# Performance work log

Hardware: AMD Instinct MI355X
Metric: run time of the kernel (lower is better)

The kernel has to match this reference:

```python
import jax, jax.numpy as jnp
import numpy as np

N, D, H, E_RAW = 100000, 128, 8, 1600000
C = D // H  # head dim = 16
NEG_SLOPE = 0.2
LN_EPS = 1e-5


def _glorot(key, shape):
    fan_in, fan_out = shape[0], shape[-1]
    lim = (6.0 / (fan_in + fan_out)) ** 0.5
    return jax.random.uniform(key, shape, jnp.float32, -lim, lim)


def setup_inputs() -> dict:
    key = jax.random.key(0)
    ks = jax.random.split(key, 16)
    inp = {
        "x": jax.random.normal(ks[0], (N, D), jnp.float32),
        "edge_index": jax.random.randint(ks[1], (2, E_RAW), 0, N, jnp.int64),
    }
    for l in range(2):
        o = 2 + 4 * l
        inp[f"Wl{l}"] = _glorot(ks[o + 0], (D, H * C))
        inp[f"Wr{l}"] = _glorot(ks[o + 1], (D, H * C))
        inp[f"att{l}"] = _glorot(ks[o + 2], (H, C))
        inp[f"b{l}"] = jnp.zeros((H * C,), jnp.float32)
        inp[f"g{l}"] = jnp.ones((D,), jnp.float32)
        inp[f"beta{l}"] = jnp.zeros((D,), jnp.float32)
    return inp


def _gatv2_layer(x, src, dst, Wl, Wr, att, b):
    # GATv2Conv: e_ij = att . leaky_relu(Wl x_j + Wr x_i); softmax over j -> i
    xl = (x @ Wl).reshape(N, H, C)  # source transform
    xr = (x @ Wr).reshape(N, H, C)  # target transform
    m = jax.nn.leaky_relu(xl[src] + xr[dst], NEG_SLOPE)  # [E,H,C]
    e = jnp.einsum("ehc,hc->eh", m, att)  # [E,H]
    emax = jax.ops.segment_max(e, dst, num_segments=N)[dst]
    ex = jnp.exp(e - emax)
    denom = jax.ops.segment_sum(ex, dst, num_segments=N)[dst]
    alpha = ex / denom  # per-destination softmax
    out = jax.ops.segment_sum(xl[src] * alpha[:, :, None], dst, num_segments=N)
    return out.reshape(N, H * C) + b


def _layernorm(x, g, beta):
    mu = jnp.mean(x, axis=-1, keepdims=True)
    var = jnp.var(x, axis=-1, keepdims=True)
    return (x - mu) * jax.lax.rsqrt(var + LN_EPS) * g + beta


def reference(x, edge_index, Wl0, Wr0, att0, b0, g0, beta0,
              Wl1, Wr1, att1, b1, g1, beta1):
    # add_self_loops=True (PyG default): every node attends to itself
    loop = jnp.arange(N, dtype=edge_index.dtype)
    src = jnp.concatenate([edge_index[0], loop])
    dst = jnp.concatenate([edge_index[1], loop])
    params = [(Wl0, Wr0, att0, b0, g0, beta0), (Wl1, Wr1, att1, b1, g1, beta1)]
    for Wl, Wr, att, b, g, beta in params:
        residual = x
        h = _gatv2_layer(x, src, dst, Wl, Wr, att, b)  # dropout is identity (eval)
        h = jax.nn.elu(h)
        x = _layernorm(h + residual, g, beta)
    return x
```

## Files before the change

### kernel.cpp

```cpp
#include <hip/hip_runtime.h>
#include <cstdint>

#define LEAKY 0.2f
#define LN_EPS 1e-5f

typedef __attribute__((ext_vector_type(8))) short short8;
typedef __attribute__((ext_vector_type(4))) float f32x4;
typedef __attribute__((ext_vector_type(2))) float f32x2;

__device__ __forceinline__ ushort bf16_rne(float x) {
    unsigned u = __float_as_uint(x);
    unsigned r = (u + 0x7fffu + ((u >> 16) & 1u)) >> 16;
    return (ushort)r;
}
__device__ __forceinline__ float bf16_to_f(ushort h) {
    return __uint_as_float(((unsigned)h) << 16);
}
__device__ __forceinline__ f32x2 unpk(uint u) {
    f32x2 r;
    r.x = __uint_as_float(u << 16);
    r.y = __uint_as_float(u & 0xffff0000u);
    return r;
}
__device__ __forceinline__ uint cvt_pk_bf16(float lo, float hi) {
    uint r;
    asm("v_cvt_pk_bf16_f32 %0, %1, %2" : "=v"(r) : "v"(lo), "v"(hi));
    return r;
}
template <int CTRL>
__device__ __forceinline__ float dpp_radd(float v) {
    int sh = __builtin_amdgcn_update_dpp(0, __float_as_int(v), CTRL, 0xF, 0xF, true);
    return v + __int_as_float(sh);
}

__global__ void hist_part(const int* __restrict__ ei, int er, int etot, int n,
                          int* __restrict__ deg) {
    const int xcd = blockIdx.x & 7;
    const int lo = (int)((long long)n * xcd >> 3);
    const int hi = (int)((long long)n * (xcd + 1) >> 3);
    const int stride = (gridDim.x >> 3) * blockDim.x;
    for (int e = (blockIdx.x >> 3) * blockDim.x + threadIdx.x; e < etot;
         e += stride) {
        int dst = (e < er) ? ei[er + e] : (e - er);
        if (dst >= lo && dst < hi) atomicAdd(&deg[dst], 1);
    }
}

__global__ void fill_part(const int* __restrict__ ei, int er, int etot, int n,
                          int* __restrict__ offs, int* __restrict__ colv) {
    const int xcd = blockIdx.x & 7;
    const int lo = (int)((long long)n * xcd >> 3);
    const int hi = (int)((long long)n * (xcd + 1) >> 3);
    const int stride = (gridDim.x >> 3) * blockDim.x;
    for (int e = (blockIdx.x >> 3) * blockDim.x + threadIdx.x; e < etot;
         e += stride) {
        int dst = (e < er) ? ei[er + e] : (e - er);
        if (dst >= lo && dst < hi) {
            int src = (e < er) ? ei[e] : dst;
            int pos = atomicAdd(&offs[dst], 1);
            colv[pos] = src;
        }
    }
}

__global__ __launch_bounds__(1024) void scanA(const int* __restrict__ deg,
                                              int* __restrict__ escan,
                                              int* __restrict__ bsum, int n) {
    __shared__ int wsum[16], wpre[16];
    const int lane = threadIdx.x & 63, wv = threadIdx.x >> 6;
    const int i = blockIdx.x * 1024 + threadIdx.x;
    int v = (i < n) ? deg[i] : 0;
    int x = v;
#pragma unroll
    for (int off = 1; off < 64; off <<= 1) {
        int y = __shfl_up(x, off, 64);
        if (lane >= off) x += y;
    }
    if (lane == 63) wsum[wv] = x;
    __syncthreads();
    if (wv == 0) {
        int s = (lane < 16) ? wsum[lane] : 0;
#pragma unroll
        for (int off = 1; off < 16; off <<= 1) {
            int y = __shfl_up(s, off, 64);
            if (lane >= off) s += y;
        }
        if (lane < 16) wpre[lane] = s;
    }
    __syncthreads();
    int excl = x - v + (wv ? wpre[wv - 1] : 0);
    if (i < n) escan[i] = excl;
    if (threadIdx.x == 1023) bsum[blockIdx.x] = wpre[15];
}

__global__ __launch_bounds__(1024) void scanB(const int* __restrict__ bsum,
                                              int* __restrict__ bpre, int nb) {
    __shared__ int wsum[16], wpre[16];
    const int lane = threadIdx.x & 63, wv = threadIdx.x >> 6;
    const int i = threadIdx.x;
    int v = (i < nb) ? bsum[i] : 0;
    int x = v;
#pragma unroll
    for (int off = 1; off < 64; off <<= 1) {
        int y = __shfl_up(x, off, 64);
        if (lane >= off) x += y;
    }
    if (lane == 63) wsum[wv] = x;
    __syncthreads();
    if (wv == 0) {
        int s = (lane < 16) ? wsum[lane] : 0;
#pragma unroll
        for (int off = 1; off < 16; off <<= 1) {
            int y = __shfl_up(s, off, 64);
            if (lane >= off) s += y;
        }
        if (lane < 16) wpre[lane] = s;
    }
    __syncthreads();
    if (i < nb) bpre[i] = x - v + (wv ? wpre[wv - 1] : 0);
}

__global__ void scanC(const int* __restrict__ escan, const int* __restrict__ bpre,
                      int* __restrict__ offs, int n) {
    int i = blockIdx.x * 256 + threadIdx.x;
    if (i >= n) return;
    offs[i] = escan[i] + bpre[i >> 10];
}

__global__ void cvt_w2(const float* __restrict__ Wl0, const float* __restrict__ Wr0,
                       const float* __restrict__ Wl1, const float* __restrict__ Wr1,
                       ushort* __restrict__ Whi, ushort* __restrict__ Wlo) {
    int t = blockIdx.x * 256 + threadIdx.x;
    int layer = t >> 15;
    int i = t & 32767;
    int colblk = i >> 11;
    int ks = (i >> 9) & 3;
    int lane = (i >> 3) & 63;
    int j = i & 7;
    int col = colblk * 16 + (lane & 15);
    int k = ks * 32 + (lane >> 4) * 8 + j;
    const float* Wl = layer ? Wl1 : Wl0;
    const float* Wr = layer ? Wr1 : Wr0;
    float v = (col < 128) ? Wl[(size_t)k * 128 + col]
                          : Wr[(size_t)k * 128 + (col - 128)];
    ushort h = bf16_rne(v);
    Whi[t] = h;
    Wlo[t] = bf16_rne(v - bf16_to_f(h));
}

template <bool ABF16>
__global__ __launch_bounds__(256) void gemm_mfma(
    const void* __restrict__ Xin,
    const ushort* __restrict__ Wfhi, const ushort* __restrict__ Wflo,
    uint* __restrict__ Olb, uint* __restrict__ Orb, int nrows) {
    __shared__ float4 xs[64 * 32];
    const int t = threadIdx.x;
    const int wave = t >> 6, lane = t & 63;
    const int m0 = blockIdx.x * 64;
    if (ABF16) {
        const uint4* Xv = (const uint4*)Xin + (size_t)m0 * 16;
        uint4* xsb = (uint4*)xs;
#pragma unroll
        for (int i = 0; i < 4; ++i) {
            int idx = i * 256 + t;
            int row = idx >> 4, kc = idx & 15;
            uint4 v = {0u, 0u, 0u, 0u};
            if (m0 + row < nrows) v = Xv[idx];
            xsb[row * 16 + (kc ^ (row & 7))] = v;
        }
    } else {
        const float4* Xv = (const float4*)Xin + (size_t)m0 * 32;
#pragma unroll
        for (int i = 0; i < 8; ++i) {
            int idx = i * 256 + t;
            int row = idx >> 5, kc = idx & 31;
            float4 v = {0.f, 0.f, 0.f, 0.f};
            if (m0 + row < nrows) v = Xv[idx];
            xs[row * 32 + (kc ^ (row & 7))] = v;
        }
    }
    __syncthreads();

    const int lrow = lane & 15;
    const int lkc = (lane >> 4) * 2;
    f32x4 acc[4][4];
#pragma unroll
    for (int mt = 0; mt < 4; ++mt)
#pragma unroll
        for (int nt = 0; nt < 4; ++nt) acc[mt][nt] = (f32x4){0.f, 0.f, 0.f, 0.f};

#pragma unroll 1
    for (int ks = 0; ks < 4; ++ks) {
        short8 bhi[4], blo[4];
#pragma unroll
        for (int nt = 0; nt < 4; ++nt) {
            size_t off = (((size_t)(wave * 4 + nt) * 4 + ks) * 64 + lane) * 8;
            bhi[nt] = *(const short8*)&Wfhi[off];
            blo[nt] = *(const short8*)&Wflo[off];
        }
        short8 ahi[4];
#pragma unroll
        for (int mt = 0; mt < 4; ++mt) {
            const int row = mt * 16 + lrow;
            if (ABF16) {
                const int slot = ks * 4 + (lane >> 4);
                uint4 w = ((const uint4*)xs)[row * 16 + (slot ^ (row & 7))];
                ahi[mt] = *(const short8*)&w;
            } else {
                const int kc0 = ks * 8 + lkc;
                float4 v0 = xs[row * 32 + (kc0 ^ (row & 7))];
                float4 v1 = xs[row * 32 + ((kc0 + 1) ^ (row & 7))];
                uint4 q;
                q.x = cvt_pk_bf16(v0.x, v0.y);
                q.y = cvt_pk_bf16(v0.z, v0.w);
                q.z = cvt_pk_bf16(v1.x, v1.y);
                q.w = cvt_pk_bf16(v1.z, v1.w);
                ahi[mt] = *(const short8*)&q;
            }
        }
#pragma unroll
        for (int nt = 0; nt < 4; ++nt) {
#pragma unroll
            for (int mt = 0; mt < 4; ++mt) {
                acc[mt][nt] = __builtin_amdgcn_mfma_f32_16x16x32_bf16(
                    ahi[mt], blo[nt], acc[mt][nt], 0, 0, 0);
                acc[mt][nt] = __builtin_amdgcn_mfma_f32_16x16x32_bf16(
                    ahi[mt], bhi[nt], acc[mt][nt], 0, 0, 0);
            }
        }
    }
    uint* __restrict__ O = (wave < 2) ? Olb : Orb;
    const int cbase = (wave * 64) & 127;
    const int crow0 = (lane >> 4) * 4;
    const bool evn = (lane & 1) == 0;
#pragma unroll
    for (int mt = 0; mt < 4; ++mt) {
#pragma unroll
        for (int i = 0; i < 4; ++i) {
            const int row = m0 + mt * 16 + crow0 + i;
#pragma unroll
            for (int nt = 0; nt < 4; ++nt) {
                float val = acc[mt][nt][i];
                float pv = __shfl_xor(val, 1);
                uint pk = (uint)bf16_rne(val) | ((uint)bf16_rne(pv) << 16);
                if (evn && row < nrows) {
                    const int col = cbase + nt * 16 + lrow;
                    O[(size_t)row * 64 + (col >> 1)] = pk;
                }
            }
        }
    }
}

template <bool RBF16, bool OBF16>
__global__ __launch_bounds__(256) void gat_agg(
    const uint* __restrict__ xl, const uint* __restrict__ xr,
    const int* __restrict__ offs, const int* __restrict__ colv,
    const float* __restrict__ att,
    const float* __restrict__ bias, const float* __restrict__ gamma,
    const float* __restrict__ beta, const void* __restrict__ resid,
    void* __restrict__ out, int nnode) {
    const int lane = threadIdx.x & 63;
    const int wid = __builtin_amdgcn_readfirstlane(threadIdx.x >> 6);
    const int wave0 = blockIdx.x * 4 + wid;
    const int wstride = gridDim.x * 4;
    const f32x2 att2 = ((const f32x2*)att)[lane];
    const f32x2 b2 = ((const f32x2*)bias)[lane];
    const f32x2 g2 = ((const f32x2*)gamma)[lane];
    const f32x2 be2 = ((const f32x2*)beta)[lane];
    for (int gid = wave0; gid < nnode; gid += wstride) {
        const uint xru = __builtin_nontemporal_load(xr + (size_t)gid * 64 + lane);
        const f32x2 xr2 = unpk(xru);
        float den = 0.f;
        f32x2 acc = {0.f, 0.f};
        int e = gid ? offs[gid - 1] : 0;
        const int e1 = offs[gid];
        for (; e + 4 <= e1; e += 4) {
            int s[4];
#pragma unroll
            for (int k = 0; k < 4; ++k)
                s[k] = __builtin_amdgcn_readfirstlane(colv[e + k]);
            uint u[4];
#pragma unroll
            for (int k = 0; k < 4; ++k) u[k] = xl[(size_t)s[k] * 64 + lane];
#pragma unroll
            for (int k = 0; k < 4; ++k) {
                f32x2 a = unpk(u[k]);
                f32x2 m = a + xr2;
                f32x2 l = m * LEAKY;
                m.x = fmaxf(m.x, l.x); m.y = fmaxf(m.y, l.y);
                f32x2 t = m * att2;
                float p = t.x + t.y;
                p = dpp_radd<0xB1>(p);
                p = dpp_radd<0x4E>(p);
                p = dpp_radd<0x141>(p);
                float ex = __expf(p);
                den += ex;
                acc += a * ex;
            }
        }
        for (; e < e1; ++e) {
            int s0 = __builtin_amdgcn_readfirstlane(colv[e]);
            uint u0 = xl[(size_t)s0 * 64 + lane];
            f32x2 a0 = unpk(u0);
            f32x2 m0 = a0 + xr2;
            f32x2 l0 = m0 * LEAKY;
            m0.x = fmaxf(m0.x, l0.x); m0.y = fmaxf(m0.y, l0.y);
            f32x2 t0 = m0 * att2;
            float p0 = t0.x + t0.y;
            p0 = dpp_radd<0xB1>(p0);
            p0 = dpp_radd<0x4E>(p0);
            p0 = dpp_radd<0x141>(p0);
            float ex0 = __expf(p0);
            den += ex0;
            acc += a0 * ex0;
        }
        const float inv_den = 1.f / den;
        f32x2 v = acc * inv_den + b2;
        v.x = v.x > 0.f ? v.x : expm1f(v.x);
        v.y = v.y > 0.f ? v.y : expm1f(v.y);
        f32x2 r2;
        if (RBF16) {
            uint ru = __builtin_nontemporal_load(
                (const uint*)resid + (size_t)gid * 64 + lane);
            r2 = unpk(ru);
        } else {
            r2 = __builtin_nontemporal_load(
                (const f32x2*)resid + (size_t)gid * 64 + lane);
        }
        f32x2 tv = v + r2;
        float s = tv.x + tv.y, ss = tv.x * tv.x + tv.y * tv.y;
        s = dpp_radd<0xB1>(s);   ss = dpp_radd<0xB1>(ss);
        s = dpp_radd<0x4E>(s);   ss = dpp_radd<0x4E>(ss);
        s = dpp_radd<0x141>(s);  ss = dpp_radd<0x141>(ss);
        s = dpp_radd<0x140>(s);  ss = dpp_radd<0x140>(ss);
        s += __shfl_xor(s, 16);  ss += __shfl_xor(ss, 16);
        s += __shfl_xor(s, 32);  ss += __shfl_xor(ss, 32);
        const float mu = s * 0.0078125f;
        const float var = ss * 0.0078125f - mu * mu;
        const float iv = rsqrtf(var + LN_EPS);
        f32x2 o = (tv - mu) * iv * g2 + be2;
        if (OBF16) {
            uint po = (uint)bf16_rne(o.x) | ((uint)bf16_rne(o.y) << 16);
            __builtin_nontemporal_store(po, (uint*)out + (size_t)gid * 64 + lane);
        } else {
            __builtin_nontemporal_store(o, (f32x2*)out + (size_t)gid * 64 + lane);
        }
    }
}

extern "C" void kernel_launch(void* const* d_in, const int* in_sizes, int n_in,
                              void* d_out, int out_size, void* d_ws, size_t ws_size,
                              hipStream_t stream) {
    const float* x   = (const float*)d_in[0];
    const int*   ei  = (const int*)d_in[1];
    const float* Wl0 = (const float*)d_in[2];
    const float* Wr0 = (const float*)d_in[3];
    const float* at0 = (const float*)d_in[4];
    const float* b0  = (const float*)d_in[5];
    const float* g0  = (const float*)d_in[6];
    const float* be0 = (const float*)d_in[7];
    const float* Wl1 = (const float*)d_in[8];
    const float* Wr1 = (const float*)d_in[9];
    const float* at1 = (const float*)d_in[10];
    const float* b1  = (const float*)d_in[11];
    const float* g1  = (const float*)d_in[12];
    const float* be1 = (const float*)d_in[13];

    const int NF = in_sizes[0];
    const int n  = NF / 128;
    const int er = in_sizes[1] / 2;
    const int etot = er + n;
    const int nb = (n + 1023) / 1024;

    uint* A     = (uint*)d_ws;
    uint* B     = A + (size_t)NF / 2;
    uint* C1    = B + (size_t)NF / 2;
    ushort* Whi = (ushort*)(C1 + (size_t)NF / 2);
    ushort* Wlo = Whi + 65536;
    int* deg    = (int*)(Wlo + 65536);
    int* offs   = deg + n;
    int* escan  = offs + (n + 4);
    int* bsum   = escan + n;
    int* bpre   = bsum + 1024;
    int* colv   = bpre + 1024;
    float* C    = (float*)d_out;

    (void)hipMemsetAsync(deg, 0, (size_t)n * sizeof(int), stream);
    hist_part<<<2048, 256, 0, stream>>>(ei, er, etot, n, deg);
    scanA<<<nb, 1024, 0, stream>>>(deg, escan, bsum, n);
    scanB<<<1, 1024, 0, stream>>>(bsum, bpre, nb);
    scanC<<<(n + 255) / 256, 256, 0, stream>>>(escan, bpre, offs, n);
    fill_part<<<2048, 256, 0, stream>>>(ei, er, etot, n, offs, colv);
    cvt_w2<<<256, 256, 0, stream>>>(Wl0, Wr0, Wl1, Wr1, Whi, Wlo);

    const int gblk = (n + 63) / 64;

    gemm_mfma<false><<<gblk, 256, 0, stream>>>(x, Whi, Wlo, A, B, n);
    gat_agg<false, true><<<2048, 256, 0, stream>>>(
        A, B, offs, colv, at0, b0, g0, be0, x, C1, n);
    gemm_mfma<true><<<gblk, 256, 0, stream>>>(C1, Whi + 32768, Wlo + 32768,
                                              A, B, n);
    gat_agg<true, false><<<2048, 256, 0, stream>>>(
        A, B, offs, colv, at1, b1, g1, be1, C1, C, n);
}
```

Measured before the change: 449.0 us.

## Split each wave into two half-waves processing different edges in the aggregation kernel

The GAT aggregation kernel now has each 32-lane half-wave cover the full 128-feature row with 4 features per lane. The two halves process different neighbor edges at once, two per half per iteration, using 8-byte gathers. Partial softmax sums are combined across halves with a cross-half shuffle at the end, and one half writes the output. This doubles the number of edge gathers in flight per wave and shortens the per-edge dot-product reduction. The costs are masked work on tail iterations, extra cross-half shuffles, and idle lanes during the store.

```diff
diff --git a/kernel.cpp b/kernel.cpp
--- a/kernel.cpp
+++ b/kernel.cpp
@@ -7,6 +7,7 @@
 typedef __attribute__((ext_vector_type(8))) short short8;
 typedef __attribute__((ext_vector_type(4))) float f32x4;
 typedef __attribute__((ext_vector_type(2))) float f32x2;
+typedef __attribute__((ext_vector_type(2))) uint u32x2;
 
 __device__ __forceinline__ ushort bf16_rne(float x) {
     unsigned u = __float_as_uint(x);
@@ -16,10 +17,12 @@
 __device__ __forceinline__ float bf16_to_f(ushort h) {
     return __uint_as_float(((unsigned)h) << 16);
 }
-__device__ __forceinline__ f32x2 unpk(uint u) {
-    f32x2 r;
-    r.x = __uint_as_float(u << 16);
-    r.y = __uint_as_float(u & 0xffff0000u);
+__device__ __forceinline__ f32x4 unpk4(u32x2 u) {
+    f32x4 r;
+    r.x = __uint_as_float(u.x << 16);
+    r.y = __uint_as_float(u.x & 0xffff0000u);
+    r.z = __uint_as_float(u.y << 16);
+    r.w = __uint_as_float(u.y & 0xffff0000u);
     return r;
 }
 __device__ __forceinline__ uint cvt_pk_bf16(float lo, float hi) {
@@ -261,90 +264,100 @@
     const float* __restrict__ beta, const void* __restrict__ resid,
     void* __restrict__ out, int nnode) {
     const int lane = threadIdx.x & 63;
+    const int hl = lane & 31;
+    const int half = lane >> 5;
     const int wid = __builtin_amdgcn_readfirstlane(threadIdx.x >> 6);
     const int wave0 = blockIdx.x * 4 + wid;
     const int wstride = gridDim.x * 4;
-    const f32x2 att2 = ((const f32x2*)att)[lane];
-    const f32x2 b2 = ((const f32x2*)bias)[lane];
-    const f32x2 g2 = ((const f32x2*)gamma)[lane];
-    const f32x2 be2 = ((const f32x2*)beta)[lane];
+    const f32x4 att4 = ((const f32x4*)att)[hl];
+    const f32x4 b4 = ((const f32x4*)bias)[hl];
+    const f32x4 g4 = ((const f32x4*)gamma)[hl];
+    const f32x4 be4 = ((const f32x4*)beta)[hl];
+    const u32x2* __restrict__ xl2 = (const u32x2*)xl;
     for (int gid = wave0; gid < nnode; gid += wstride) {
-        const uint xru = __builtin_nontemporal_load(xr + (size_t)gid * 64 + lane);
-        const f32x2 xr2 = unpk(xru);
+        const u32x2 xru = __builtin_nontemporal_load(
+            (const u32x2*)xr + (size_t)gid * 32 + hl);
+        const f32x4 xr4 = unpk4(xru);
         float den = 0.f;
-        f32x2 acc = {0.f, 0.f};
+        f32x4 acc = {0.f, 0.f, 0.f, 0.f};
         int e = gid ? offs[gid - 1] : 0;
         const int e1 = offs[gid];
-        for (; e + 4 <= e1; e += 4) {
-            int s[4];
-#pragma unroll
-            for (int k = 0; k < 4; ++k)
-                s[k] = __builtin_amdgcn_readfirstlane(colv[e + k]);
-            uint u[4];
-#pragma unroll
-            for (int k = 0; k < 4; ++k) u[k] = xl[(size_t)s[k] * 64 + lane];
-#pragma unroll
-            for (int k = 0; k < 4; ++k) {
-                f32x2 a = unpk(u[k]);
-                f32x2 m = a + xr2;
-                f32x2 l = m * LEAKY;
-                m.x = fmaxf(m.x, l.x); m.y = fmaxf(m.y, l.y);
-                f32x2 t = m * att2;
-                float p = t.x + t.y;
-                p = dpp_radd<0xB1>(p);
-                p = dpp_radd<0x4E>(p);
-                p = dpp_radd<0x141>(p);
-                float ex = __expf(p);
-                den += ex;
-                acc += a * ex;
-            }
-        }
-        for (; e < e1; ++e) {
+        const int e1m = e1 - 1;
+        for (; e < e1; e += 4) {
             int s0 = __builtin_amdgcn_readfirstlane(colv[e]);
-            uint u0 = xl[(size_t)s0 * 64 + lane];
-            f32x2 a0 = unpk(u0);
-            f32x2 m0 = a0 + xr2;
-            f32x2 l0 = m0 * LEAKY;
-            m0.x = fmaxf(m0.x, l0.x); m0.y = fmaxf(m0.y, l0.y);
-            f32x2 t0 = m0 * att2;
-            float p0 = t0.x + t0.y;
-            p0 = dpp_radd<0xB1>(p0);
-            p0 = dpp_radd<0x4E>(p0);
-            p0 = dpp_radd<0x141>(p0);
-            float ex0 = __expf(p0);
-            den += ex0;
-            acc += a0 * ex0;
-        }
+            int s1 = __builtin_amdgcn_readfirstlane(colv[min(e + 1, e1m)]);
+            int s2 = __builtin_amdgcn_readfirstlane(colv[min(e + 2, e1m)]);
+            int s3 = __builtin_amdgcn_readfirstlane(colv[min(e + 3, e1m)]);
+            int selA = half ? s1 : s0;
+            int selB = half ? s3 : s2;
+            u32x2 uA = xl2[(size_t)selA * 32 + hl];
+            u32x2 uB = xl2[(size_t)selB * 32 + hl];
+            f32x4 aA = unpk4(uA);
+            f32x4 mA = aA + xr4;
+            mA.x = fmaxf(mA.x, LEAKY * mA.x); mA.y = fmaxf(mA.y, LEAKY * mA.y);
+            mA.z = fmaxf(mA.z, LEAKY * mA.z); mA.w = fmaxf(mA.w, LEAKY * mA.w);
+            f32x4 tA = mA * att4;
+            float pA = (tA.x + tA.y) + (tA.z + tA.w);
+            pA = dpp_radd<0xB1>(pA);
+            pA = dpp_radd<0x4E>(pA);
+            float exA = (e + half < e1) ? __expf(pA) : 0.f;
+            den += exA;
+            acc += aA * exA;
+            f32x4 aB = unpk4(uB);
+            f32x4 mB = aB + xr4;
+            mB.x = fmaxf(mB.x, LEAKY * mB.x); mB.y = fmaxf(mB.y, LEAKY * mB.y);
+            mB.z = fmaxf(mB.z, LEAKY * mB.z); mB.w = fmaxf(mB.w, LEAKY * mB.w);
+            f32x4 tB = mB * att4;
+            float pB = (tB.x + tB.y) + (tB.z + tB.w);
+            pB = dpp_radd<0xB1>(pB);
+            pB = dpp_radd<0x4E>(pB);
+            float exB = (e + 2 + half < e1) ? __expf(pB) : 0.f;
+            den += exB;
+            acc += aB * exB;
+        }
+        den += __shfl_xor(den, 32);
+        acc.x += __shfl_xor(acc.x, 32);
+        acc.y += __shfl_xor(acc.y, 32);
+        acc.z += __shfl_xor(acc.z, 32);
+        acc.w += __shfl_xor(acc.w, 32);
         const float inv_den = 1.f / den;
-        f32x2 v = acc * inv_den + b2;
+        f32x4 v = acc * inv_den + b4;
         v.x = v.x > 0.f ? v.x : expm1f(v.x);
         v.y = v.y > 0.f ? v.y : expm1f(v.y);
-        f32x2 r2;
+        v.z = v.z > 0.f ? v.z : expm1f(v.z);
+        v.w = v.w > 0.f ? v.w : expm1f(v.w);
+        f32x4 r4;
         if (RBF16) {
-            uint ru = __builtin_nontemporal_load(
-                (const uint*)resid + (size_t)gid * 64 + lane);
-            r2 = unpk(ru);
+            u32x2 ru = __builtin_nontemporal_load(
+                (const u32x2*)resid + (size_t)gid * 32 + hl);
+            r4 = unpk4(ru);
         } else {
-            r2 = __builtin_nontemporal_load(
-                (const f32x2*)resid + (size_t)gid * 64 + lane);
-        }
-        f32x2 tv = v + r2;
-        float s = tv.x + tv.y, ss = tv.x * tv.x + tv.y * tv.y;
+            r4 = __builtin_nontemporal_load(
+                (const f32x4*)resid + (size_t)gid * 32 + hl);
+        }
+        f32x4 tv = v + r4;
+        float s = (tv.x + tv.y) + (tv.z + tv.w);
+        float ss = (tv.x * tv.x + tv.y * tv.y) + (tv.z * tv.z + tv.w * tv.w);
         s = dpp_radd<0xB1>(s);   ss = dpp_radd<0xB1>(ss);
         s = dpp_radd<0x4E>(s);   ss = dpp_radd<0x4E>(ss);
         s = dpp_radd<0x141>(s);  ss = dpp_radd<0x141>(ss);
         s = dpp_radd<0x140>(s);  ss = dpp_radd<0x140>(ss);
         s += __shfl_xor(s, 16);  ss += __shfl_xor(ss, 16);
-        s += __shfl_xor(s, 32);  ss += __shfl_xor(ss, 32);
         const float mu = s * 0.0078125f;
         const float var = ss * 0.0078125f - mu * mu;
         const float iv = rsqrtf(var + LN_EPS);
-        f32x2 o = (tv - mu) * iv * g2 + be2;
-        if (OBF16) {
-            uint po = (uint)bf16_rne(o.x) | ((uint)bf16_rne(o.y) << 16);
-            __builtin_nontemporal_store(po, (uint*)out + (size_t)gid * 64 + lane);
-        } else {
-            __builtin_nontemporal_store(o, (f32x2*)out + (size_t)gid * 64 + lane);
+        f32x4 o = (tv - mu) * iv * g4 + be4;
+        if (half == 0) {
+            if (OBF16) {
+                u32x2 po;
+                po.x = (uint)bf16_rne(o.x) | ((uint)bf16_rne(o.y) << 16);
+                po.y = (uint)bf16_rne(o.z) | ((uint)bf16_rne(o.w) << 16);
+                __builtin_nontemporal_store(
+                    po, (u32x2*)out + (size_t)gid * 32 + hl);
+            } else {
+                __builtin_nontemporal_store(
+                    o, (f32x4*)out + (size_t)gid * 32 + hl);
+            }
         }
     }
 }
```

New measurement: 468.5 us. 1.04x slower.
